# Optimization experiments

Measured on AMD Instinct MI355X. Metric: run time of the kernel, lower is better.

## Reference

```python
import jax, jax.numpy as jnp
import numpy as np

N_NODES = 100000
N_EDGES = 1600000
D = 128
N_LAYERS = 3


def setup_inputs() -> dict:
    key = jax.random.key(0)
    ks = jax.random.split(key, 6)
    x = jax.random.normal(ks[0], (N_NODES, D), dtype=jnp.float32)
    edge_index = jax.random.randint(ks[1], (2, N_EDGES), 0, N_NODES, dtype=jnp.int64)
    # GIN MLP params per layer: Linear(D,D) -> ReLU -> Linear(D,D)
    W1 = jax.random.normal(ks[2], (N_LAYERS, D, D), dtype=jnp.float32) * 0.05
    b1 = jnp.zeros((N_LAYERS, D), dtype=jnp.float32)
    W2 = jax.random.normal(ks[3], (N_LAYERS, D, D), dtype=jnp.float32) * 0.05
    b2 = jnp.zeros((N_LAYERS, D), dtype=jnp.float32)
    return {"x": x, "edge_index": edge_index, "W1": W1, "b1": b1, "W2": W2, "b2": b2}


def reference(x, edge_index, W1, b1, W2, b2):
    # MultiscaleEncoder with conv='GIN', conv_dropout=0 (dropout skipped).
    # GINConv (eps=0): out = MLP(x + sum_{src->dst} x[src]), aggregated at dst.
    src, dst = edge_index[0], edge_index[1]
    n = x.shape[0]
    outs = []
    for l in range(W1.shape[0]):
        agg = jax.ops.segment_sum(x[src], dst, num_segments=n)  # [N, D]
        h = x + agg  # (1 + eps) * x + agg with eps = 0
        h = jax.nn.relu(h @ W1[l] + b1[l])
        h = h @ W2[l] + b2[l]
        x = jax.nn.relu(h)  # per-layer ReLU in MultiscaleEncoder.forward
        outs.append(x)
    return jnp.stack(outs)  # [n_layers, N, D]
```

## Files before the change

### kernel.cpp

```cpp
#include <hip/hip_runtime.h>

#define D 128
#define MAXDEG 64

typedef __attribute__((ext_vector_type(8))) short bf16x8;
typedef __attribute__((ext_vector_type(4))) float f32x4;

__device__ inline unsigned short f2b(float f) {
    union { float f; unsigned int u; } v; v.f = f;
    unsigned int u = v.u;
    u += 0x7fffu + ((u >> 16) & 1u);
    return (unsigned short)(u >> 16);
}
__device__ inline float bl(unsigned int u) { union { unsigned int u; float f; } c; c.u = u << 16; return c.f; }
__device__ inline float bh(unsigned int u) { union { unsigned int u; float f; } c; c.u = u & 0xffff0000u; return c.f; }

__global__ void detect_and_zero(const int* __restrict__ ei, int E, int* __restrict__ flag,
                                int* __restrict__ deg, int n) {
    int tid = blockIdx.x * blockDim.x + threadIdx.x;
    for (int i = tid; i < n; i += gridDim.x * blockDim.x) deg[i] = 0;
    if (tid == 0) {
        int z = 0;
        int nprobe = (E > 32) ? 32 : E;
        for (int i = 0; i < nprobe; i++) z |= ei[2 * i + 1];
        flag[0] = (z == 0) ? 1 : 0;
    }
}

__global__ void fill_slots_part(const int* __restrict__ ei, int E, int n,
                                const int* __restrict__ flag,
                                int* __restrict__ deg, int* __restrict__ slots) {
    int grp = blockIdx.x & 7;
    int per = n >> 3;
    int r0 = grp * per;
    int r1 = (grp == 7) ? n : r0 + per;
    int m = flag[0];
    int tpg = (gridDim.x >> 3) * blockDim.x;
    int idx = (blockIdx.x >> 3) * blockDim.x + threadIdx.x;
    for (int i = idx; i < E; i += tpg) {
        int d = m ? ei[2 * (E + i)] : ei[E + i];
        if (d >= r0 && d < r1) {
            int s = m ? ei[2 * i] : ei[i];
            int pos = atomicAdd(&deg[d], 1);
            if (pos < MAXDEG) slots[(size_t)d * MAXDEG + pos] = s;
        }
    }
}

__global__ void conv_wx(const float* __restrict__ W1, const float* __restrict__ W2,
                        unsigned short* __restrict__ Wt, int L,
                        const float* __restrict__ x, unsigned short* __restrict__ xb,
                        int total4) {
    int i = blockIdx.x * blockDim.x + threadIdx.x;
    int totalW = L * 2 * D * D;
    if (i < totalW) {
        int l = i / (2 * D * D);
        int rem = i - l * 2 * D * D;
        int which = rem / (D * D);
        int idx = rem - which * D * D;
        int c = idx >> 7, k = idx & 127;
        const float* W = which ? W2 : W1;
        Wt[i] = f2b(W[(size_t)l * D * D + k * D + c]);
    } else if (xb) {
        int j = i - totalW;
        if (j < total4) {
            float4 v = ((const float4*)x)[j];
            uint2 o;
            o.x = (unsigned int)f2b(v.x) | ((unsigned int)f2b(v.y) << 16);
            o.y = (unsigned int)f2b(v.z) | ((unsigned int)f2b(v.w) << 16);
            ((uint2*)xb)[j] = o;
        }
    }
}

__global__ void agg_bf16(const unsigned short* __restrict__ xb, const int* __restrict__ slots,
                         const int* __restrict__ deg, unsigned short* __restrict__ A, int n) {
    int node = blockIdx.x * (blockDim.x >> 6) + (threadIdx.x >> 6);
    if (node >= n) return;
    int lane = threadIdx.x & 63;
    int q = lane >> 4, l16 = lane & 15;
    const uint4* xv = (const uint4*)xb;

    float a0 = 0.f, a1 = 0.f, a2 = 0.f, a3 = 0.f;
    float a4 = 0.f, a5 = 0.f, a6 = 0.f, a7 = 0.f;
    if (q == 0) {
        uint4 sv = xv[(size_t)node * 16 + l16];
        a0 += bl(sv.x); a1 += bh(sv.x); a2 += bl(sv.y); a3 += bh(sv.y);
        a4 += bl(sv.z); a5 += bh(sv.z); a6 += bl(sv.w); a7 += bh(sv.w);
    }
    int dg = deg[node]; if (dg > MAXDEG) dg = MAXDEG;
    int beg = node * MAXDEG;
    int end = beg + dg;
    int i = beg + q;
    for (; i + 12 < end; i += 16) {
        int s0 = slots[i], s1 = slots[i + 4], s2 = slots[i + 8], s3 = slots[i + 12];
        uint4 v0 = xv[(size_t)s0 * 16 + l16];
        uint4 v1 = xv[(size_t)s1 * 16 + l16];
        uint4 v2 = xv[(size_t)s2 * 16 + l16];
        uint4 v3 = xv[(size_t)s3 * 16 + l16];
        a0 += bl(v0.x); a1 += bh(v0.x); a2 += bl(v0.y); a3 += bh(v0.y);
        a4 += bl(v0.z); a5 += bh(v0.z); a6 += bl(v0.w); a7 += bh(v0.w);
        a0 += bl(v1.x); a1 += bh(v1.x); a2 += bl(v1.y); a3 += bh(v1.y);
        a4 += bl(v1.z); a5 += bh(v1.z); a6 += bl(v1.w); a7 += bh(v1.w);
        a0 += bl(v2.x); a1 += bh(v2.x); a2 += bl(v2.y); a3 += bh(v2.y);
        a4 += bl(v2.z); a5 += bh(v2.z); a6 += bl(v2.w); a7 += bh(v2.w);
        a0 += bl(v3.x); a1 += bh(v3.x); a2 += bl(v3.y); a3 += bh(v3.y);
        a4 += bl(v3.z); a5 += bh(v3.z); a6 += bl(v3.w); a7 += bh(v3.w);
    }
    for (; i < end; i += 4) {
        int s0 = slots[i];
        uint4 v0 = xv[(size_t)s0 * 16 + l16];
        a0 += bl(v0.x); a1 += bh(v0.x); a2 += bl(v0.y); a3 += bh(v0.y);
        a4 += bl(v0.z); a5 += bh(v0.z); a6 += bl(v0.w); a7 += bh(v0.w);
    }
    a0 += __shfl_xor(a0, 16); a1 += __shfl_xor(a1, 16);
    a2 += __shfl_xor(a2, 16); a3 += __shfl_xor(a3, 16);
    a4 += __shfl_xor(a4, 16); a5 += __shfl_xor(a5, 16);
    a6 += __shfl_xor(a6, 16); a7 += __shfl_xor(a7, 16);
    a0 += __shfl_xor(a0, 32); a1 += __shfl_xor(a1, 32);
    a2 += __shfl_xor(a2, 32); a3 += __shfl_xor(a3, 32);
    a4 += __shfl_xor(a4, 32); a5 += __shfl_xor(a5, 32);
    a6 += __shfl_xor(a6, 32); a7 += __shfl_xor(a7, 32);
    if (q == 0) {
        uint4 o;
        o.x = (unsigned int)f2b(a0) | ((unsigned int)f2b(a1) << 16);
        o.y = (unsigned int)f2b(a2) | ((unsigned int)f2b(a3) << 16);
        o.z = (unsigned int)f2b(a4) | ((unsigned int)f2b(a5) << 16);
        o.w = (unsigned int)f2b(a6) | ((unsigned int)f2b(a7) << 16);
        ((uint4*)A)[(size_t)node * 16 + l16] = o;
    }
}

__global__ void agg_f32(const float* __restrict__ x, const int* __restrict__ slots,
                        const int* __restrict__ deg, unsigned short* __restrict__ A, int n) {
    int node = blockIdx.x * (blockDim.x >> 6) + (threadIdx.x >> 6);
    if (node >= n) return;
    int d2 = threadIdx.x & 63;
    const float2* xr = (const float2*)(x + (size_t)node * D);
    float2 acc = xr[d2];
    int dg = deg[node]; if (dg > MAXDEG) dg = MAXDEG;
    int beg = node * MAXDEG, end = beg + dg;
    for (int i = beg; i < end; i++) {
        int s = slots[i];
        float2 v = ((const float2*)(x + (size_t)s * D))[d2];
        acc.x += v.x; acc.y += v.y;
    }
    unsigned int pk = (unsigned int)f2b(acc.x) | ((unsigned int)f2b(acc.y) << 16);
    ((unsigned int*)(A + (size_t)node * D))[d2] = pk;
}

__global__ __launch_bounds__(256) void mlp_fused(
    const unsigned short* __restrict__ Ain,
    const unsigned short* __restrict__ Wt1,
    const unsigned short* __restrict__ Wt2,
    const float* __restrict__ b1, const float* __restrict__ b2,
    int n, float* __restrict__ outF, unsigned short* __restrict__ outXB) {

    __shared__ unsigned char Hs[128 * 256];

    int wave = threadIdx.x >> 6;
    int lane = threadIdx.x & 63;
    int l16 = lane & 15, g = lane >> 4;
    int rowbase = blockIdx.x * 128 + wave * 32;

    f32x4 acc[2][8];
    #pragma unroll
    for (int rf = 0; rf < 2; rf++)
        #pragma unroll
        for (int cf = 0; cf < 8; cf++)
            acc[rf][cf] = (f32x4){0.f, 0.f, 0.f, 0.f};

    #pragma unroll
    for (int ks = 0; ks < 4; ks++) {
        int k0 = ks * 32 + g * 8;
        bf16x8 a[2];
        #pragma unroll
        for (int rf = 0; rf < 2; rf++) {
            int row = rowbase + rf * 16 + l16;
            if (row >= n) row = n - 1;
            a[rf] = *((const bf16x8*)(Ain + (size_t)row * D + k0));
        }
        #pragma unroll
        for (int cf = 0; cf < 8; cf++) {
            int col = cf * 16 + l16;
            bf16x8 b = *((const bf16x8*)(Wt1 + col * D + k0));
            acc[0][cf] = __builtin_amdgcn_mfma_f32_16x16x32_bf16(a[0], b, acc[0][cf], 0, 0, 0);
            acc[1][cf] = __builtin_amdgcn_mfma_f32_16x16x32_bf16(a[1], b, acc[1][cf], 0, 0, 0);
        }
    }

    #pragma unroll
    for (int cf = 0; cf < 8; cf++) {
        int col = cf * 16 + l16;
        float bv = b1[col];
        #pragma unroll
        for (int rf = 0; rf < 2; rf++) {
            #pragma unroll
            for (int r = 0; r < 4; r++) {
                int rl = wave * 32 + rf * 16 + g * 4 + r;
                float v = acc[rf][cf][r] + bv;
                v = (v < 0.f) ? 0.f : v;
                int byte = (rl * 256 + col * 2) ^ ((rl & 7) << 4);
                *(unsigned short*)(Hs + byte) = f2b(v);
            }
        }
    }
    __syncthreads();

    f32x4 acc2[2][8];
    #pragma unroll
    for (int rf = 0; rf < 2; rf++)
        #pragma unroll
        for (int cf = 0; cf < 8; cf++)
            acc2[rf][cf] = (f32x4){0.f, 0.f, 0.f, 0.f};

    #pragma unroll
    for (int ks = 0; ks < 4; ks++) {
        int k0 = ks * 32 + g * 8;
        bf16x8 a[2];
        #pragma unroll
        for (int rf = 0; rf < 2; rf++) {
            int rl = wave * 32 + rf * 16 + l16;
            int byte = (rl * 256 + k0 * 2) ^ ((rl & 7) << 4);
            a[rf] = *(const bf16x8*)(Hs + byte);
        }
        #pragma unroll
        for (int cf = 0; cf < 8; cf++) {
            int col = cf * 16 + l16;
            bf16x8 b = *((const bf16x8*)(Wt2 + col * D + k0));
            acc2[0][cf] = __builtin_amdgcn_mfma_f32_16x16x32_bf16(a[0], b, acc2[0][cf], 0, 0, 0);
            acc2[1][cf] = __builtin_amdgcn_mfma_f32_16x16x32_bf16(a[1], b, acc2[1][cf], 0, 0, 0);
        }
    }

    #pragma unroll
    for (int cf = 0; cf < 8; cf++) {
        int col = cf * 16 + l16;
        float bv = b2[col];
        #pragma unroll
        for (int rf = 0; rf < 2; rf++) {
            #pragma unroll
            for (int r = 0; r < 4; r++) {
                int row = rowbase + rf * 16 + g * 4 + r;
                if (row < n) {
                    float v = acc2[rf][cf][r] + bv;
                    v = (v < 0.f) ? 0.f : v;
                    __builtin_nontemporal_store(v, &outF[(size_t)row * D + col]);
                    if (outXB) outXB[(size_t)row * D + col] = f2b(v);
                }
            }
        }
    }
}

extern "C" void kernel_launch(void* const* d_in, const int* in_sizes, int n_in,
                              void* d_out, int out_size, void* d_ws, size_t ws_size,
                              hipStream_t stream) {
    const float* x  = (const float*)d_in[0];
    const int*   ei = (const int*)d_in[1];
    const float* W1 = (const float*)d_in[2];
    const float* b1 = (const float*)d_in[3];
    const float* W2 = (const float*)d_in[4];
    const float* b2 = (const float*)d_in[5];
    float* out = (float*)d_out;

    int N = in_sizes[0] / D;
    int E = in_sizes[1] / 2;
    int L = in_sizes[3] / D;

    auto alignup = [](size_t v) { return (v + 255) & ~(size_t)255; };
    size_t sz_flag  = 256;
    size_t sz_deg   = alignup((size_t)N * 4);
    size_t sz_slots = alignup((size_t)N * MAXDEG * 4);
    size_t sz_wt    = alignup((size_t)L * 2 * D * D * 2);
    size_t sz_mat   = alignup((size_t)N * D * 2);
    size_t base = sz_flag + sz_deg + sz_slots + sz_wt + sz_mat;
    bool useBf16 = (base + sz_mat) <= ws_size;

    char* p = (char*)d_ws;
    int* flag   = (int*)p;             p += sz_flag;
    int* deg    = (int*)p;             p += sz_deg;
    int* slots  = (int*)p;             p += sz_slots;
    unsigned short* Wt = (unsigned short*)p; p += sz_wt;
    unsigned short* A  = (unsigned short*)p; p += sz_mat;
    unsigned short* XB = (unsigned short*)p;

    detect_and_zero<<<512, 256, 0, stream>>>(ei, E, flag, deg, N);
    fill_slots_part<<<2048, 256, 0, stream>>>(ei, E, N, flag, deg, slots);

    int totalW = L * 2 * D * D;
    int total4 = N * D / 4;
    int convTot = totalW + (useBf16 ? total4 : 0);
    conv_wx<<<(convTot + 255) / 256, 256, 0, stream>>>(
        W1, W2, Wt, L, x, useBf16 ? XB : nullptr, total4);

    for (int l = 0; l < L; l++) {
        if (useBf16) {
            agg_bf16<<<(N + 3) / 4, 256, 0, stream>>>(XB, slots, deg, A, N);
        } else {
            const float* xin = (l == 0) ? x : out + (size_t)(l - 1) * N * D;
            agg_f32<<<(N + 3) / 4, 256, 0, stream>>>(xin, slots, deg, A, N);
        }
        unsigned short* nextXB = (useBf16 && l + 1 < L) ? XB : nullptr;
        mlp_fused<<<(N + 127) / 128, 256, 0, stream>>>(
            A, Wt + (size_t)l * 2 * D * D, Wt + (size_t)l * 2 * D * D + D * D,
            b1 + (size_t)l * D, b2 + (size_t)l * D, N,
            out + (size_t)l * N * D, nextXB);
    }
}
```

Baseline: 468.0 us.

## Merge preprocessing kernels and vectorize neighbor slot loads in aggregation

```diff
diff --git a/kernel.cpp b/kernel.cpp
--- a/kernel.cpp
+++ b/kernel.cpp
@@ -5,6 +5,7 @@
 
 typedef __attribute__((ext_vector_type(8))) short bf16x8;
 typedef __attribute__((ext_vector_type(4))) float f32x4;
+typedef __attribute__((ext_vector_type(4))) unsigned int u32x4;
 
 __device__ inline unsigned short f2b(float f) {
     union { float f; unsigned int u; } v; v.f = f;
@@ -15,10 +16,34 @@
 __device__ inline float bl(unsigned int u) { union { unsigned int u; float f; } c; c.u = u << 16; return c.f; }
 __device__ inline float bh(unsigned int u) { union { unsigned int u; float f; } c; c.u = u & 0xffff0000u; return c.f; }
 
-__global__ void detect_and_zero(const int* __restrict__ ei, int E, int* __restrict__ flag,
-                                int* __restrict__ deg, int n) {
+__global__ void pre_kernel(const int* __restrict__ ei, int E, int* __restrict__ flag,
+                           int* __restrict__ deg, int n,
+                           const float* __restrict__ W1, const float* __restrict__ W2,
+                           unsigned short* __restrict__ Wt, int L,
+                           const float* __restrict__ x, unsigned short* __restrict__ xb,
+                           int total4) {
     int tid = blockIdx.x * blockDim.x + threadIdx.x;
-    for (int i = tid; i < n; i += gridDim.x * blockDim.x) deg[i] = 0;
+    int stride = gridDim.x * blockDim.x;
+    for (int i = tid; i < n; i += stride) deg[i] = 0;
+    int totalW = L * 2 * D * D;
+    for (int i = tid; i < totalW; i += stride) {
+        int l = i / (2 * D * D);
+        int rem = i - l * 2 * D * D;
+        int which = rem / (D * D);
+        int idx = rem - which * D * D;
+        int c = idx >> 7, k = idx & 127;
+        const float* W = which ? W2 : W1;
+        Wt[i] = f2b(W[(size_t)l * D * D + k * D + c]);
+    }
+    if (xb) {
+        for (int j = tid; j < total4; j += stride) {
+            float4 v = ((const float4*)x)[j];
+            uint2 o;
+            o.x = (unsigned int)f2b(v.x) | ((unsigned int)f2b(v.y) << 16);
+            o.y = (unsigned int)f2b(v.z) | ((unsigned int)f2b(v.w) << 16);
+            ((uint2*)xb)[j] = o;
+        }
+    }
     if (tid == 0) {
         int z = 0;
         int nprobe = (E > 32) ? 32 : E;
@@ -47,36 +72,11 @@
     }
 }
 
-__global__ void conv_wx(const float* __restrict__ W1, const float* __restrict__ W2,
-                        unsigned short* __restrict__ Wt, int L,
-                        const float* __restrict__ x, unsigned short* __restrict__ xb,
-                        int total4) {
-    int i = blockIdx.x * blockDim.x + threadIdx.x;
-    int totalW = L * 2 * D * D;
-    if (i < totalW) {
-        int l = i / (2 * D * D);
-        int rem = i - l * 2 * D * D;
-        int which = rem / (D * D);
-        int idx = rem - which * D * D;
-        int c = idx >> 7, k = idx & 127;
-        const float* W = which ? W2 : W1;
-        Wt[i] = f2b(W[(size_t)l * D * D + k * D + c]);
-    } else if (xb) {
-        int j = i - totalW;
-        if (j < total4) {
-            float4 v = ((const float4*)x)[j];
-            uint2 o;
-            o.x = (unsigned int)f2b(v.x) | ((unsigned int)f2b(v.y) << 16);
-            o.y = (unsigned int)f2b(v.z) | ((unsigned int)f2b(v.w) << 16);
-            ((uint2*)xb)[j] = o;
-        }
-    }
-}
-
 __global__ void agg_bf16(const unsigned short* __restrict__ xb, const int* __restrict__ slots,
                          const int* __restrict__ deg, unsigned short* __restrict__ A, int n) {
     int node = blockIdx.x * (blockDim.x >> 6) + (threadIdx.x >> 6);
     if (node >= n) return;
+    int nodeU = __builtin_amdgcn_readfirstlane(node);
     int lane = threadIdx.x & 63;
     int q = lane >> 4, l16 = lane & 15;
     const uint4* xv = (const uint4*)xb;
@@ -84,20 +84,21 @@
     float a0 = 0.f, a1 = 0.f, a2 = 0.f, a3 = 0.f;
     float a4 = 0.f, a5 = 0.f, a6 = 0.f, a7 = 0.f;
     if (q == 0) {
-        uint4 sv = xv[(size_t)node * 16 + l16];
+        uint4 sv = xv[(size_t)nodeU * 16 + l16];
         a0 += bl(sv.x); a1 += bh(sv.x); a2 += bl(sv.y); a3 += bh(sv.y);
         a4 += bl(sv.z); a5 += bh(sv.z); a6 += bl(sv.w); a7 += bh(sv.w);
     }
-    int dg = deg[node]; if (dg > MAXDEG) dg = MAXDEG;
-    int beg = node * MAXDEG;
-    int end = beg + dg;
-    int i = beg + q;
-    for (; i + 12 < end; i += 16) {
-        int s0 = slots[i], s1 = slots[i + 4], s2 = slots[i + 8], s3 = slots[i + 12];
-        uint4 v0 = xv[(size_t)s0 * 16 + l16];
-        uint4 v1 = xv[(size_t)s1 * 16 + l16];
-        uint4 v2 = xv[(size_t)s2 * 16 + l16];
-        uint4 v3 = xv[(size_t)s3 * 16 + l16];
+    int dg = deg[nodeU]; if (dg > MAXDEG) dg = MAXDEG;
+    const int* sl = slots + (size_t)nodeU * MAXDEG;
+
+    int C16 = dg & ~15;
+    int i = 4 * q;
+    for (; i < C16; i += 16) {
+        int4 ss = *(const int4*)(sl + i);
+        uint4 v0 = xv[(size_t)ss.x * 16 + l16];
+        uint4 v1 = xv[(size_t)ss.y * 16 + l16];
+        uint4 v2 = xv[(size_t)ss.z * 16 + l16];
+        uint4 v3 = xv[(size_t)ss.w * 16 + l16];
         a0 += bl(v0.x); a1 += bh(v0.x); a2 += bl(v0.y); a3 += bh(v0.y);
         a4 += bl(v0.z); a5 += bh(v0.z); a6 += bl(v0.w); a7 += bh(v0.w);
         a0 += bl(v1.x); a1 += bh(v1.x); a2 += bl(v1.y); a3 += bh(v1.y);
@@ -107,12 +108,26 @@
         a0 += bl(v3.x); a1 += bh(v3.x); a2 += bl(v3.y); a3 += bh(v3.y);
         a4 += bl(v3.z); a5 += bh(v3.z); a6 += bl(v3.w); a7 += bh(v3.w);
     }
-    for (; i < end; i += 4) {
-        int s0 = slots[i];
-        uint4 v0 = xv[(size_t)s0 * 16 + l16];
-        a0 += bl(v0.x); a1 += bh(v0.x); a2 += bl(v0.y); a3 += bh(v0.y);
-        a4 += bl(v0.z); a5 += bh(v0.z); a6 += bl(v0.w); a7 += bh(v0.w);
-    }
+    int tbase = C16 + 4 * q;
+    if (tbase < dg) {
+        int4 ss = *(const int4*)(sl + tbase);
+        {   uint4 v0 = xv[(size_t)ss.x * 16 + l16];
+            a0 += bl(v0.x); a1 += bh(v0.x); a2 += bl(v0.y); a3 += bh(v0.y);
+            a4 += bl(v0.z); a5 += bh(v0.z); a6 += bl(v0.w); a7 += bh(v0.w); }
+        if (tbase + 1 < dg) {
+            uint4 v0 = xv[(size_t)ss.y * 16 + l16];
+            a0 += bl(v0.x); a1 += bh(v0.x); a2 += bl(v0.y); a3 += bh(v0.y);
+            a4 += bl(v0.z); a5 += bh(v0.z); a6 += bl(v0.w); a7 += bh(v0.w); }
+        if (tbase + 2 < dg) {
+            uint4 v0 = xv[(size_t)ss.z * 16 + l16];
+            a0 += bl(v0.x); a1 += bh(v0.x); a2 += bl(v0.y); a3 += bh(v0.y);
+            a4 += bl(v0.z); a5 += bh(v0.z); a6 += bl(v0.w); a7 += bh(v0.w); }
+        if (tbase + 3 < dg) {
+            uint4 v0 = xv[(size_t)ss.w * 16 + l16];
+            a0 += bl(v0.x); a1 += bh(v0.x); a2 += bl(v0.y); a3 += bh(v0.y);
+            a4 += bl(v0.z); a5 += bh(v0.z); a6 += bl(v0.w); a7 += bh(v0.w); }
+    }
+
     a0 += __shfl_xor(a0, 16); a1 += __shfl_xor(a1, 16);
     a2 += __shfl_xor(a2, 16); a3 += __shfl_xor(a3, 16);
     a4 += __shfl_xor(a4, 16); a5 += __shfl_xor(a5, 16);
@@ -127,7 +142,7 @@
         o.y = (unsigned int)f2b(a2) | ((unsigned int)f2b(a3) << 16);
         o.z = (unsigned int)f2b(a4) | ((unsigned int)f2b(a5) << 16);
         o.w = (unsigned int)f2b(a6) | ((unsigned int)f2b(a7) << 16);
-        ((uint4*)A)[(size_t)node * 16 + l16] = o;
+        ((uint4*)A)[(size_t)nodeU * 16 + l16] = o;
     }
 }
 
@@ -178,7 +193,10 @@
         for (int rf = 0; rf < 2; rf++) {
             int row = rowbase + rf * 16 + l16;
             if (row >= n) row = n - 1;
-            a[rf] = *((const bf16x8*)(Ain + (size_t)row * D + k0));
+            u32x4 t = __builtin_nontemporal_load(
+                (const u32x4*)(Ain + (size_t)row * D + k0));
+            union { u32x4 u; bf16x8 v; } cvt; cvt.u = t;
+            a[rf] = cvt.v;
         }
         #pragma unroll
         for (int cf = 0; cf < 8; cf++) {
@@ -285,14 +303,10 @@
     unsigned short* A  = (unsigned short*)p; p += sz_mat;
     unsigned short* XB = (unsigned short*)p;
 
-    detect_and_zero<<<512, 256, 0, stream>>>(ei, E, flag, deg, N);
+    int total4 = N * D / 4;
+    pre_kernel<<<2048, 256, 0, stream>>>(ei, E, flag, deg, N, W1, W2, Wt, L,
+                                         x, useBf16 ? XB : nullptr, total4);
     fill_slots_part<<<2048, 256, 0, stream>>>(ei, E, N, flag, deg, slots);
-
-    int totalW = L * 2 * D * D;
-    int total4 = N * D / 4;
-    int convTot = totalW + (useBf16 ? total4 : 0);
-    conv_wx<<<(convTot + 255) / 256, 256, 0, stream>>>(
-        W1, W2, Wt, L, x, useBf16 ? XB : nullptr, total4);
 
     for (int l = 0; l < L; l++) {
         if (useBf16) {
```

After: 468.4 us (median of 2 runs). Within noise of the previous version (+0.1%).
